# Kernel tuning notes

Hardware: AMD Instinct MI355X
Metric: run time of the kernel (lower is better)

The kernel has to match this reference:

```python
import jax, jax.numpy as jnp
import numpy as np

N, M, D = 1024, 1024, 256

def setup_inputs() -> dict:
    key = jax.random.key(0)
    ks = jax.random.split(key, 10)
    s = 1.0 / np.sqrt(D)
    return {
        "f_r": jax.random.normal(ks[0], (N, D), jnp.float32),
        "f_r_prime": jax.random.normal(ks[1], (M, D), jnp.float32),
        "W_w": jax.random.uniform(ks[2], (D, D), jnp.float32, -s, s),
        "W_b": jax.random.uniform(ks[3], (D,), jnp.float32, -s, s),
        "Wp_w": jax.random.uniform(ks[4], (D, D), jnp.float32, -s, s),
        "Wp_b": jax.random.uniform(ks[5], (D,), jnp.float32, -s, s),
        "w_w": jax.random.uniform(ks[6], (1, D), jnp.float32, -s, s),
        "w_b": jax.random.uniform(ks[7], (1,), jnp.float32, -s, s),
        "wp_w": jax.random.uniform(ks[8], (1, D), jnp.float32, -s, s),
        "wp_b": jax.random.uniform(ks[9], (1,), jnp.float32, -s, s),
    }

def reference(f_r, f_r_prime, W_w, W_b, Wp_w, Wp_b, w_w, w_b, wp_w, wp_b):
    q = f_r @ W_w.T + W_b            # [N, D]
    k = f_r_prime @ Wp_w.T + Wp_b    # [M, D]
    # additive (Bahdanau) scores: tanh over broadcast sum [N, M, D]
    h = jnp.tanh(q[:, None, :] + k[None, :, :])
    alpha = h @ w_w.T + w_b          # [N, M, 1]
    alpha = jax.nn.softmax(alpha, axis=1)
    # stage-1 pooling over M (weights on raw f_r_prime, as in source)
    context = jnp.sum(alpha * f_r_prime[None, :, :], axis=1)  # [N, D]
    # stage-2 attention pooling over N
    alpha_p = jax.nn.softmax(context @ wp_w.T + wp_b, axis=0)  # [N, 1]
    pool = jnp.sum(alpha_p * context, axis=0, keepdims=True)   # [1, D]
    return pool
```

## Files before the change

kernel.cpp:

```cpp
#include <hip/hip_runtime.h>

#define NN 1024
#define MM 1024
#define DD 256

typedef float floatx2 __attribute__((ext_vector_type(2)));

__device__ __forceinline__ float rcp_fast(float x) { return __builtin_amdgcn_rcpf(x); }

__global__ __launch_bounds__(256) void gemm_exp_kernel(
    const float* __restrict__ f_r,  const float* __restrict__ W_w,  const float* __restrict__ W_b,
    const float* __restrict__ f_rp, const float* __restrict__ Wp_w, const float* __restrict__ Wp_b,
    float* __restrict__ Eq, float* __restrict__ EkT, float* __restrict__ out0)
{
    __shared__ float As[32][36];
    __shared__ float Bs[32][68];
    __shared__ float T[64][36];

    const int b = blockIdx.x;
    const int t = threadIdx.x;
    if (b == 0) out0[t] = 0.f;

    const int mat  = b >> 7;
    const int tile = b & 127;
    const int rt = tile & 31, dt = tile >> 5;
    const float* __restrict__ A    = mat ? f_rp : f_r;
    const float* __restrict__ B    = mat ? Wp_w : W_w;
    const float* __restrict__ bias = mat ? Wp_b : W_b;

    const int tx = t & 15, ty = t >> 4;
    const int r0 = rt * 32, d0 = dt * 64;
    const int ar = t >> 3, ak = (t & 7) * 4;
    const int br = t >> 2, bk = (t & 3) * 8;

    float acc[2][4];
    #pragma unroll
    for (int i = 0; i < 2; ++i)
        #pragma unroll
        for (int j = 0; j < 4; ++j) acc[i][j] = 0.f;

    for (int kk = 0; kk < DD; kk += 32) {
        float4 av  = *(const float4*)(A + (size_t)(r0 + ar) * DD + kk + ak);
        float4 bv0 = *(const float4*)(B + (size_t)(d0 + br) * DD + kk + bk);
        float4 bv1 = *(const float4*)(B + (size_t)(d0 + br) * DD + kk + bk + 4);
        __syncthreads();
        As[ak + 0][ar] = av.x; As[ak + 1][ar] = av.y; As[ak + 2][ar] = av.z; As[ak + 3][ar] = av.w;
        Bs[bk + 0][br] = bv0.x; Bs[bk + 1][br] = bv0.y; Bs[bk + 2][br] = bv0.z; Bs[bk + 3][br] = bv0.w;
        Bs[bk + 4][br] = bv1.x; Bs[bk + 5][br] = bv1.y; Bs[bk + 6][br] = bv1.z; Bs[bk + 7][br] = bv1.w;
        __syncthreads();
        #pragma unroll
        for (int k = 0; k < 32; ++k) {
            float2 a2 = *(const float2*)&As[k][ty * 2];
            float4 b4 = *(const float4*)&Bs[k][tx * 4];
            float aa[2] = {a2.x, a2.y};
            float bb[4] = {b4.x, b4.y, b4.z, b4.w};
            #pragma unroll
            for (int i = 0; i < 2; ++i)
                #pragma unroll
                for (int j = 0; j < 4; ++j)
                    acc[i][j] = fmaf(aa[i], bb[j], acc[i][j]);
        }
    }

    float bj[4];
    #pragma unroll
    for (int j = 0; j < 4; ++j) bj[j] = bias[d0 + tx * 4 + j];

    float e[2][4];
    #pragma unroll
    for (int i = 0; i < 2; ++i)
        #pragma unroll
        for (int j = 0; j < 4; ++j) {
            float v = acc[i][j] + bj[j];
            v = fminf(fmaxf(v, -5.f), 5.f);
            e[i][j] = __expf(2.f * v);
        }

    if (mat == 0) {
        #pragma unroll
        for (int i = 0; i < 2; ++i)
            *(float4*)&Eq[(size_t)(r0 + ty * 2 + i) * DD + d0 + tx * 4] =
                make_float4(e[i][0], e[i][1], e[i][2], e[i][3]);
    } else {
        __syncthreads();
        #pragma unroll
        for (int i = 0; i < 2; ++i)
            #pragma unroll
            for (int j = 0; j < 4; ++j) T[tx * 4 + j][ty * 2 + i] = e[i][j];
        __syncthreads();
        const int dl = t >> 3, rl = (t & 7) * 4;
        #pragma unroll
        for (int h = 0; h < 2; ++h) {
            int dloc = dl + 32 * h;
            float4 tv = *(const float4*)&T[dloc][rl];
            *(float4*)&EkT[(size_t)(d0 + dloc) * MM + r0 + rl] = tv;
        }
    }
}

__global__ __launch_bounds__(1024, 4) void fused_attn_kernel(
    const float* __restrict__ Eq, const float* __restrict__ EkT,
    const float* __restrict__ w_w, const float* __restrict__ frp,
    const float* __restrict__ wp_w,
    float* __restrict__ ctx, float* __restrict__ score)
{
    __shared__ float eq[4 * DD];
    __shared__ float w2[DD];
    __shared__ float accbuf[3][16][256];
    __shared__ float alsm[4][MM];
    __shared__ float4 ctxred[16][4][64];
    __shared__ float redmx[4][4];
    __shared__ float redsm[4][4];
    __shared__ float redsc[16];

    const int t  = threadIdx.x;
    const int tg = t >> 8;
    const int tm = t & 255;
    const int lane = t & 63, wid = t >> 6;
    const int n0 = blockIdx.x * 4;
    const int dh = tg * 64;

    eq[t] = Eq[(size_t)n0 * DD + t];
    if (t < DD) w2[t] = -2.0f * w_w[t];
    __syncthreads();

    const floatx2 one2 = {1.f, 1.f};
    floatx2 accl[4] = {{0.f,0.f},{0.f,0.f},{0.f,0.f},{0.f,0.f}};
    floatx2 acch[4] = {{0.f,0.f},{0.f,0.f},{0.f,0.f},{0.f,0.f}};

    const float* ekb = EkT + (size_t)dh * MM + 4 * tm;
    float4 c0 = *(const float4*)(ekb + 0 * MM);
    float4 c1 = *(const float4*)(ekb + 1 * MM);
    float4 c2 = *(const float4*)(ekb + 2 * MM);
    float4 c3 = *(const float4*)(ekb + 3 * MM);

    for (int gi = 0; gi < 16; ++gi) {
        float4 p0 = c0, p1 = c1, p2 = c2, p3 = c3;
        if (gi < 15) {
            const float* nb = ekb + (size_t)(gi * 4 + 4) * MM;
            p0 = *(const float4*)(nb + 0 * MM);
            p1 = *(const float4*)(nb + 1 * MM);
            p2 = *(const float4*)(nb + 2 * MM);
            p3 = *(const float4*)(nb + 3 * MM);
        }
        const int db = gi * 4;
        float4 w4 = *(const float4*)&w2[dh + db];
        floatx2 kv[4][2] = {{{c0.x, c0.y}, {c0.z, c0.w}},
                            {{c1.x, c1.y}, {c1.z, c1.w}},
                            {{c2.x, c2.y}, {c2.z, c2.w}},
                            {{c3.x, c3.y}, {c3.z, c3.w}}};
        #pragma unroll
        for (int n = 0; n < 4; ++n) {
            float4 q4 = *(const float4*)&eq[n * DD + dh + db];
            #pragma unroll
            for (int h = 0; h < 2; ++h) {
                floatx2 x0 = q4.x * kv[0][h] + one2;
                floatx2 x1 = q4.y * kv[1][h] + one2;
                floatx2 x2 = q4.z * kv[2][h] + one2;
                floatx2 x3 = q4.w * kv[3][h] + one2;
                floatx2 p01 = x0 * x1;
                floatx2 p23 = x2 * x3;
                floatx2 n01 = w4.x * x1 + w4.y * x0;
                floatx2 n23 = w4.z * x3 + w4.w * x2;
                floatx2 nc  = n01 * p23 + n23 * p01;
                floatx2 pt  = p01 * p23;
                floatx2 r;  r.x = rcp_fast(pt.x);  r.y = rcp_fast(pt.y);
                if (h == 0) accl[n] += nc * r; else acch[n] += nc * r;
            }
        }
        c0 = p0; c1 = p1; c2 = p2; c3 = p3;
    }

    float acc[4][4];
    #pragma unroll
    for (int n = 0; n < 4; ++n) {
        acc[n][0] = accl[n].x; acc[n][1] = accl[n].y;
        acc[n][2] = acch[n].x; acc[n][3] = acch[n].y;
    }

    if (tg > 0) {
        #pragma unroll
        for (int n = 0; n < 4; ++n)
            #pragma unroll
            for (int j = 0; j < 4; ++j) accbuf[tg - 1][n * 4 + j][tm] = acc[n][j];
    }
    __syncthreads();
    if (tg == 0) {
        #pragma unroll
        for (int s = 0; s < 3; ++s)
            #pragma unroll
            for (int n = 0; n < 4; ++n)
                #pragma unroll
                for (int j = 0; j < 4; ++j) acc[n][j] += accbuf[s][n * 4 + j][tm];
        float mx[4];
        #pragma unroll
        for (int n = 0; n < 4; ++n) {
            mx[n] = fmaxf(fmaxf(acc[n][0], acc[n][1]), fmaxf(acc[n][2], acc[n][3]));
            #pragma unroll
            for (int off = 32; off > 0; off >>= 1) mx[n] = fmaxf(mx[n], __shfl_xor(mx[n], off));
            if (lane == 0) redmx[wid][n] = mx[n];
        }
    }
    __syncthreads();
    float e[4][4];
    if (tg == 0) {
        #pragma unroll
        for (int n = 0; n < 4; ++n) {
            float MX = fmaxf(fmaxf(redmx[0][n], redmx[1][n]), fmaxf(redmx[2][n], redmx[3][n]));
            float sm = 0.f;
            #pragma unroll
            for (int j = 0; j < 4; ++j) { e[n][j] = __expf(acc[n][j] - MX); sm += e[n][j]; }
            #pragma unroll
            for (int off = 32; off > 0; off >>= 1) sm += __shfl_xor(sm, off);
            if (lane == 0) redsm[wid][n] = sm;
        }
    }
    __syncthreads();
    if (tg == 0) {
        #pragma unroll
        for (int n = 0; n < 4; ++n) {
            float S = redsm[0][n] + redsm[1][n] + redsm[2][n] + redsm[3][n];
            float inv = rcp_fast(S);
            #pragma unroll
            for (int j = 0; j < 4; ++j) alsm[n][4 * tm + j] = e[n][j] * inv;
        }
    }
    __syncthreads();

    const int cc = t & 63;
    const int rr = t >> 6;
    const int m0 = rr * 64;
    floatx2 axl[4] = {{0.f,0.f},{0.f,0.f},{0.f,0.f},{0.f,0.f}};
    floatx2 axh[4] = {{0.f,0.f},{0.f,0.f},{0.f,0.f},{0.f,0.f}};
    const float* fb = frp + (size_t)m0 * DD + 4 * cc;
    for (int m4 = 0; m4 < 16; ++m4) {
        float alv[4][4];
        #pragma unroll
        for (int n = 0; n < 4; ++n) {
            float4 a4 = *(const float4*)&alsm[n][m0 + m4 * 4];
            alv[n][0] = a4.x; alv[n][1] = a4.y; alv[n][2] = a4.z; alv[n][3] = a4.w;
        }
        #pragma unroll
        for (int mm = 0; mm < 4; ++mm) {
            float4 f = *(const float4*)(fb + (size_t)(m4 * 4 + mm) * DD);
            floatx2 fl = {f.x, f.y}, fh = {f.z, f.w};
            #pragma unroll
            for (int n = 0; n < 4; ++n) {
                axl[n] += alv[n][mm] * fl;
                axh[n] += alv[n][mm] * fh;
            }
        }
    }
    #pragma unroll
    for (int n = 0; n < 4; ++n)
        ctxred[rr][n][cc] = make_float4(axl[n].x, axl[n].y, axh[n].x, axh[n].y);
    __syncthreads();

    const int nn = t >> 8, d = t & 255;
    float s = 0.f;
    #pragma unroll
    for (int r = 0; r < 16; ++r)
        s += ((const float*)&ctxred[r][nn][d >> 2])[d & 3];
    ctx[(size_t)(n0 + nn) * DD + d] = s;

    float p = s * wp_w[d];
    #pragma unroll
    for (int off = 32; off > 0; off >>= 1) p += __shfl_xor(p, off);
    if (lane == 0) redsc[wid] = p;
    __syncthreads();
    if (t < 4) score[n0 + t] = redsc[4 * t] + redsc[4 * t + 1] + redsc[4 * t + 2] + redsc[4 * t + 3];
}

__global__ __launch_bounds__(256) void pool_kernel(
    const float* __restrict__ ctx, const float* __restrict__ score,
    float* __restrict__ out)
{
    __shared__ float red[8];
    const int t = threadIdx.x, lane = t & 63, wid = t >> 6;
    const int n0 = blockIdx.x * 4;

    float s0 = score[t], s1 = score[t + 256], s2 = score[t + 512], s3 = score[t + 768];
    float mx = fmaxf(fmaxf(s0, s1), fmaxf(s2, s3));
    #pragma unroll
    for (int off = 32; off > 0; off >>= 1) mx = fmaxf(mx, __shfl_xor(mx, off));
    if (lane == 0) red[wid] = mx;
    __syncthreads();
    mx = fmaxf(fmaxf(red[0], red[1]), fmaxf(red[2], red[3]));

    float se = __expf(s0 - mx) + __expf(s1 - mx) + __expf(s2 - mx) + __expf(s3 - mx);
    #pragma unroll
    for (int off = 32; off > 0; off >>= 1) se += __shfl_xor(se, off);
    if (lane == 0) red[4 + wid] = se;
    __syncthreads();
    se = red[4] + red[5] + red[6] + red[7];
    float invS = rcp_fast(se);

    float r = 0.f;
    #pragma unroll
    for (int i = 0; i < 4; ++i) {
        float ap = __expf(score[n0 + i] - mx) * invS;
        r = fmaf(ap, ctx[(size_t)(n0 + i) * DD + t], r);
    }
    atomicAdd(out + t, r);
}

extern "C" void kernel_launch(void* const* d_in, const int* in_sizes, int n_in,
                              void* d_out, int out_size, void* d_ws, size_t ws_size,
                              hipStream_t stream) {
    const float* f_r  = (const float*)d_in[0];
    const float* f_rp = (const float*)d_in[1];
    const float* W_w  = (const float*)d_in[2];
    const float* W_b  = (const float*)d_in[3];
    const float* Wp_w = (const float*)d_in[4];
    const float* Wp_b = (const float*)d_in[5];
    const float* w_w  = (const float*)d_in[6];
    const float* wp_w = (const float*)d_in[8];
    float* out = (float*)d_out;

    float* ws    = (float*)d_ws;
    float* Eq    = ws;
    float* EkT   = ws + 262144;
    float* ctx   = ws + 524288;
    float* score = ws + 786432;

    gemm_exp_kernel<<<256, 256, 0, stream>>>(f_r, W_w, W_b, f_rp, Wp_w, Wp_b, Eq, EkT, out);
    fused_attn_kernel<<<256, 1024, 0, stream>>>(Eq, EkT, w_w, f_rp, wp_w, ctx, score);
    pool_kernel<<<256, 256, 0, stream>>>(ctx, score, out);
}
```

Before: 125.1 us.

## Spread softmax over all thread groups and read Eq/w_w directly from global

The softmax reduction is spread across all four 256-thread groups, one per query row, instead of running only in group 0 after the others spill partials. All four groups now write partials to a larger shared buffer and each sums its own row, and the -2 scale is applied after accumulation rather than folded into a prescaled w_w copy. The shared staging of Eq and w_w, and the sync that followed it, is removed; these operands are now read from global/scalar memory with a wave-uniform offset. This removes idle threads in the softmax phase and one barrier, at the cost of more shared memory for accbuf and uncached global loads inside the hot loop.

```diff
diff --git a/kernel.cpp b/kernel.cpp
--- a/kernel.cpp
+++ b/kernel.cpp
@@ -104,9 +104,7 @@
     const float* __restrict__ wp_w,
     float* __restrict__ ctx, float* __restrict__ score)
 {
-    __shared__ float eq[4 * DD];
-    __shared__ float w2[DD];
-    __shared__ float accbuf[3][16][256];
+    __shared__ float accbuf[4][16][256];
     __shared__ float alsm[4][MM];
     __shared__ float4 ctxred[16][4][64];
     __shared__ float redmx[4][4];
@@ -116,13 +114,11 @@
     const int t  = threadIdx.x;
     const int tg = t >> 8;
     const int tm = t & 255;
-    const int lane = t & 63, wid = t >> 6;
     const int n0 = blockIdx.x * 4;
-    const int dh = tg * 64;
-
-    eq[t] = Eq[(size_t)n0 * DD + t];
-    if (t < DD) w2[t] = -2.0f * w_w[t];
-    __syncthreads();
+
+    const int dh = __builtin_amdgcn_readfirstlane(tg * 64);
+    const float* __restrict__ eqb = Eq + (size_t)n0 * DD + dh;
+    const float* __restrict__ wwb = w_w + dh;
 
     const floatx2 one2 = {1.f, 1.f};
     floatx2 accl[4] = {{0.f,0.f},{0.f,0.f},{0.f,0.f},{0.f,0.f}};
@@ -144,14 +140,14 @@
             p3 = *(const float4*)(nb + 3 * MM);
         }
         const int db = gi * 4;
-        float4 w4 = *(const float4*)&w2[dh + db];
+        float4 w4 = *(const float4*)(wwb + db);
         floatx2 kv[4][2] = {{{c0.x, c0.y}, {c0.z, c0.w}},
                             {{c1.x, c1.y}, {c1.z, c1.w}},
                             {{c2.x, c2.y}, {c2.z, c2.w}},
                             {{c3.x, c3.y}, {c3.z, c3.w}}};
         #pragma unroll
         for (int n = 0; n < 4; ++n) {
-            float4 q4 = *(const float4*)&eq[n * DD + dh + db];
+            float4 q4 = *(const float4*)(eqb + n * DD + db);
             #pragma unroll
             for (int h = 0; h < 2; ++h) {
                 floatx2 x0 = q4.x * kv[0][h] + one2;
@@ -174,57 +170,42 @@
     float acc[4][4];
     #pragma unroll
     for (int n = 0; n < 4; ++n) {
-        acc[n][0] = accl[n].x; acc[n][1] = accl[n].y;
-        acc[n][2] = acch[n].x; acc[n][3] = acch[n].y;
-    }
-
-    if (tg > 0) {
-        #pragma unroll
-        for (int n = 0; n < 4; ++n)
-            #pragma unroll
-            for (int j = 0; j < 4; ++j) accbuf[tg - 1][n * 4 + j][tm] = acc[n][j];
-    }
-    __syncthreads();
-    if (tg == 0) {
-        #pragma unroll
-        for (int s = 0; s < 3; ++s)
-            #pragma unroll
-            for (int n = 0; n < 4; ++n)
-                #pragma unroll
-                for (int j = 0; j < 4; ++j) acc[n][j] += accbuf[s][n * 4 + j][tm];
-        float mx[4];
-        #pragma unroll
-        for (int n = 0; n < 4; ++n) {
-            mx[n] = fmaxf(fmaxf(acc[n][0], acc[n][1]), fmaxf(acc[n][2], acc[n][3]));
-            #pragma unroll
-            for (int off = 32; off > 0; off >>= 1) mx[n] = fmaxf(mx[n], __shfl_xor(mx[n], off));
-            if (lane == 0) redmx[wid][n] = mx[n];
-        }
-    }
-    __syncthreads();
-    float e[4][4];
-    if (tg == 0) {
-        #pragma unroll
-        for (int n = 0; n < 4; ++n) {
-            float MX = fmaxf(fmaxf(redmx[0][n], redmx[1][n]), fmaxf(redmx[2][n], redmx[3][n]));
-            float sm = 0.f;
-            #pragma unroll
-            for (int j = 0; j < 4; ++j) { e[n][j] = __expf(acc[n][j] - MX); sm += e[n][j]; }
-            #pragma unroll
-            for (int off = 32; off > 0; off >>= 1) sm += __shfl_xor(sm, off);
-            if (lane == 0) redsm[wid][n] = sm;
-        }
-    }
-    __syncthreads();
-    if (tg == 0) {
-        #pragma unroll
-        for (int n = 0; n < 4; ++n) {
-            float S = redsm[0][n] + redsm[1][n] + redsm[2][n] + redsm[3][n];
-            float inv = rcp_fast(S);
-            #pragma unroll
-            for (int j = 0; j < 4; ++j) alsm[n][4 * tm + j] = e[n][j] * inv;
-        }
-    }
+        acc[n][0] = -2.f * accl[n].x; acc[n][1] = -2.f * accl[n].y;
+        acc[n][2] = -2.f * acch[n].x; acc[n][3] = -2.f * acch[n].y;
+    }
+
+    #pragma unroll
+    for (int n = 0; n < 4; ++n)
+        #pragma unroll
+        for (int j = 0; j < 4; ++j) accbuf[tg][n * 4 + j][tm] = acc[n][j];
+    __syncthreads();
+
+    const int g = tg;
+    const int w4id = (t >> 6) & 3;
+    const int lane = t & 63;
+    float aj[4];
+    #pragma unroll
+    for (int j = 0; j < 4; ++j)
+        aj[j] = accbuf[0][g * 4 + j][tm] + accbuf[1][g * 4 + j][tm]
+              + accbuf[2][g * 4 + j][tm] + accbuf[3][g * 4 + j][tm];
+
+    float mx = fmaxf(fmaxf(aj[0], aj[1]), fmaxf(aj[2], aj[3]));
+    #pragma unroll
+    for (int off = 32; off > 0; off >>= 1) mx = fmaxf(mx, __shfl_xor(mx, off));
+    if (lane == 0) redmx[g][w4id] = mx;
+    __syncthreads();
+    const float MX = fmaxf(fmaxf(redmx[g][0], redmx[g][1]), fmaxf(redmx[g][2], redmx[g][3]));
+
+    float e[4], sm = 0.f;
+    #pragma unroll
+    for (int j = 0; j < 4; ++j) { e[j] = __expf(aj[j] - MX); sm += e[j]; }
+    #pragma unroll
+    for (int off = 32; off > 0; off >>= 1) sm += __shfl_xor(sm, off);
+    if (lane == 0) redsm[g][w4id] = sm;
+    __syncthreads();
+    const float S = redsm[g][0] + redsm[g][1] + redsm[g][2] + redsm[g][3];
+    const float inv = rcp_fast(S);
+    *(float4*)&alsm[g][4 * tm] = make_float4(e[0] * inv, e[1] * inv, e[2] * inv, e[3] * inv);
     __syncthreads();
 
     const int cc = t & 63;
@@ -266,7 +247,7 @@
     float p = s * wp_w[d];
     #pragma unroll
     for (int off = 32; off > 0; off >>= 1) p += __shfl_xor(p, off);
-    if (lane == 0) redsc[wid] = p;
+    if (lane == 0) redsc[t >> 6] = p;
     __syncthreads();
     if (t < 4) score[n0 + t] = redsc[4 * t] + redsc[4 * t + 1] + redsc[4 * t + 2] + redsc[4 * t + 3];
 }
```

After: 122.8 us. About the same (-1.8%).
